# Kernel optimization log

Measured on AMD Instinct MI355X. Metric: run time of the kernel, lower is better.

The kernel has to match this reference:

```python
import jax, jax.numpy as jnp
import numpy as np

B, IN, N, OUT = 65536, 512, 256, 64  # batch, in_size, neurons, out_size


def setup_inputs() -> dict:
    key = jax.random.key(0)
    k1, k2, k3, k4 = jax.random.split(key, 4)
    return {
        "x": jax.random.normal(k1, (B, IN), jnp.float32),
        "W_lin": jax.random.normal(k2, (IN, N + OUT), jnp.float32),   # nlinear
        "W_nl": jax.random.normal(k3, (N - 1, N), jnp.float32),        # padded nonlinear[i] rows
        "W_out": jax.random.normal(k4, (OUT, N), jnp.float32),         # output_weights[0:out_size]
    }


def reference(x, W_lin, W_nl, W_out):
    act = jnp.tanh
    lin = x @ W_lin  # [B, N+OUT]
    # row i of nonlinear weights is valid only for entries 0..i (length i+1)
    tri_mask = (jnp.arange(N)[None, :] <= jnp.arange(N - 1)[:, None]).astype(lin.dtype)
    Wm = W_nl * tri_mask  # [N-1, N]
    # growing accumulator, fixed-size buffer; position 0 = lin[0] + 1
    acc0 = jnp.zeros((x.shape[0], N), lin.dtype).at[:, 0].set(lin[:, 0] + 1.0)
    col = jnp.arange(N)[None, :]

    def step(acc, inp):
        w, l, i = inp  # w: [N] masked weights, l: [B] = lin[:, i], i: scalar step
        v = jnp.sum(act(acc) * w[None, :], axis=1) + l + 1.0  # [B]
        acc = jnp.where(col == (i + 1), v[:, None], acc)
        return acc, None

    xs = (Wm, lin[:, : N - 1].T, jnp.arange(N - 1))
    acc, _ = jax.lax.scan(step, acc0, xs)
    # outs[i] = act(t) @ output_weights[i] + lin[neurons + i] + 1
    out = act(acc) @ W_out.T + lin[:, N:] + 1.0  # [B, OUT]
    return out
```

## Files before the change

kernel.cpp:

```cpp
#include <hip/hip_runtime.h>
#include <hip/hip_bf16.h>

typedef _Float16 f16x8 __attribute__((ext_vector_type(8)));
typedef unsigned short u16x8 __attribute__((ext_vector_type(8)));
typedef float f32x4 __attribute__((ext_vector_type(4)));
typedef unsigned int u32x4 __attribute__((ext_vector_type(4)));

static __device__ __forceinline__ unsigned short h2u(_Float16 h) {
    return __builtin_bit_cast(unsigned short, h);
}
static __device__ __forceinline__ float fast_tanh(float x) {
    float e = __expf(2.0f * x);
    return 1.0f - 2.0f / (e + 1.0f);
}

__global__ void cascade_prep(const float* __restrict__ W_lin,
                             const float* __restrict__ W_nl,
                             const float* __restrict__ W_out,
                             unsigned short* __restrict__ wlin_h,
                             unsigned short* __restrict__ wlin_l,
                             unsigned short* __restrict__ wnl_h,
                             unsigned short* __restrict__ wnl_l,
                             unsigned short* __restrict__ wout_h,
                             unsigned short* __restrict__ wout_l,
                             float* __restrict__ wcol) {
    int idx = blockIdx.x * blockDim.x + threadIdx.x;
    int stride = gridDim.x * blockDim.x;
    for (int i = idx; i < 320 * 512; i += stride) {
        int n = i >> 9, k = i & 511;
        float w = W_lin[k * 320 + n];
        _Float16 h = (_Float16)w;
        wlin_h[i] = h2u(h);
        wlin_l[i] = h2u((_Float16)(w - (float)h));
    }
    for (int i = idx; i < 255 * 256; i += stride) {
        int r = i >> 8, k = i & 255;
        float w = (k <= r) ? W_nl[i] : 0.0f;
        _Float16 h = (_Float16)w;
        wnl_h[i] = h2u(h);
        wnl_l[i] = h2u((_Float16)(w - (float)h));
    }
    for (int i = idx; i < 64 * 256; i += stride) {
        float w = W_out[i];
        _Float16 h = (_Float16)w;
        wout_h[i] = h2u(h);
        wout_l[i] = h2u((_Float16)(w - (float)h));
    }
    for (int i = idx; i < 256; i += stride) {
        int b = i >> 5, u = i & 31;
        float* dst = wcol + b * 496 + (31 * u - (u * (u - 1)) / 2);
        for (int j = u + 1; j < 32; ++j)
            dst[j - u - 1] = W_nl[(size_t)(b * 32 + j - 1) * 256 + b * 32 + u];
    }
}

__global__ __launch_bounds__(512, 1) void lin_gemm(
    const float* __restrict__ x,
    const unsigned short* __restrict__ wlin_h,
    const unsigned short* __restrict__ wlin_l,
    float* __restrict__ linc,
    float* __restrict__ lino) {

    __shared__ _Float16 bufH[2][16 * 520];
    __shared__ _Float16 bufL[2][16 * 520];

    const int tid = threadIdx.x;
    const int wv  = tid >> 6;
    const int l15 = tid & 15;
    const int g   = (tid & 63) >> 4;
    const int s = (blockIdx.x & 7) * 64 + (blockIdx.x >> 3);
    const long row0 = (long)s * 128;

    f16x8 xfh[16], xfl[16];
    {
        const float* xp = x + (row0 + wv * 16 + l15) * 512 + g * 8;
        #pragma unroll
        for (int ks = 0; ks < 16; ++ks) {
            float4 p0 = *reinterpret_cast<const float4*>(xp + ks * 32);
            float4 p1 = *reinterpret_cast<const float4*>(xp + ks * 32 + 4);
            float av[8] = {p0.x, p0.y, p0.z, p0.w, p1.x, p1.y, p1.z, p1.w};
            f16x8 fh, fl;
            #pragma unroll
            for (int e = 0; e < 8; ++e) {
                _Float16 hh = (_Float16)av[e];
                fh[e] = hh;
                fl[e] = (_Float16)(av[e] - (float)hh);
            }
            xfh[ks] = fh;
            xfl[ks] = fl;
        }
    }

    u16x8 rh[2], rl[2];
    #define STAGE_LOAD(nt)                                                     \
        {                                                                      \
            _Pragma("unroll")                                                  \
            for (int it = 0; it < 2; ++it) {                                   \
                int flat = it * 4096 + tid * 8;                                \
                int r = flat >> 9, c = flat & 511;                             \
                rh[it] = *reinterpret_cast<const u16x8*>(                      \
                    wlin_h + (size_t)((nt) * 16 + r) * 512 + c);               \
                rl[it] = *reinterpret_cast<const u16x8*>(                      \
                    wlin_l + (size_t)((nt) * 16 + r) * 512 + c);               \
            }                                                                  \
        }
    #define STAGE_WRITE(buf)                                                   \
        {                                                                      \
            _Pragma("unroll")                                                  \
            for (int it = 0; it < 2; ++it) {                                   \
                int flat = it * 4096 + tid * 8;                                \
                int r = flat >> 9, c = flat & 511;                             \
                *reinterpret_cast<u16x8*>(&bufH[buf][r * 520 + c]) =           \
                    __builtin_bit_cast(u16x8, rh[it]);                         \
                *reinterpret_cast<u16x8*>(&bufL[buf][r * 520 + c]) =           \
                    __builtin_bit_cast(u16x8, rl[it]);                         \
            }                                                                  \
        }

    STAGE_LOAD(0);
    STAGE_WRITE(0);
    __syncthreads();

    int cur = 0;
    for (int nt = 0; nt < 20; ++nt) {
        if (nt < 19) STAGE_LOAD(nt + 1);

        f32x4 acc = (f32x4){0.f, 0.f, 0.f, 0.f};
        if (nt < 16) {
            #pragma unroll
            for (int ks = 0; ks < 16; ++ks) {
                f16x8 bh = *reinterpret_cast<const f16x8*>(
                    &bufH[cur][l15 * 520 + ks * 32 + g * 8]);
                f16x8 bl = *reinterpret_cast<const f16x8*>(
                    &bufL[cur][l15 * 520 + ks * 32 + g * 8]);
                acc = __builtin_amdgcn_mfma_f32_16x16x32_f16(xfh[ks], bh, acc, 0, 0, 0);
                acc = __builtin_amdgcn_mfma_f32_16x16x32_f16(xfl[ks], bh, acc, 0, 0, 0);
                acc = __builtin_amdgcn_mfma_f32_16x16x32_f16(xfh[ks], bl, acc, 0, 0, 0);
            }
            int c = nt * 16 + l15;
            #pragma unroll
            for (int j = 0; j < 4; ++j) {
                long row = row0 + wv * 16 + g * 4 + j;
                if (c < 255) linc[row * 256 + c + 1] = acc[j];
                if (c == 0)  linc[row * 256] = acc[j];
            }
        } else {
            #pragma unroll
            for (int ks = 0; ks < 16; ++ks) {
                f16x8 bh = *reinterpret_cast<const f16x8*>(
                    &bufH[cur][l15 * 520 + ks * 32 + g * 8]);
                acc = __builtin_amdgcn_mfma_f32_16x16x32_f16(xfh[ks], bh, acc, 0, 0, 0);
            }
            #pragma unroll
            for (int j = 0; j < 4; ++j)
                lino[(row0 + wv * 16 + g * 4 + j) * 64 + (nt - 16) * 16 + l15] = acc[j];
        }

        if (nt < 19) STAGE_WRITE(cur ^ 1);
        __syncthreads();
        cur ^= 1;
    }
    #undef STAGE_LOAD
    #undef STAGE_WRITE
}

static __device__ __forceinline__ void unpack_pf(u32x4 a0, u32x4 a1,
                                                 f16x8* ah, f16x8* al) {
    u32x4 hx, lx;
    hx[0] = (a0[0] & 0xffffu) | (a0[1] << 16);
    hx[1] = (a0[2] & 0xffffu) | (a0[3] << 16);
    hx[2] = (a1[0] & 0xffffu) | (a1[1] << 16);
    hx[3] = (a1[2] & 0xffffu) | (a1[3] << 16);
    lx[0] = (a0[0] >> 16) | (a0[1] & 0xffff0000u);
    lx[1] = (a0[2] >> 16) | (a0[3] & 0xffff0000u);
    lx[2] = (a1[0] >> 16) | (a1[1] & 0xffff0000u);
    lx[3] = (a1[2] >> 16) | (a1[3] & 0xffff0000u);
    *ah = __builtin_bit_cast(f16x8, hx);
    *al = __builtin_bit_cast(f16x8, lx);
}

__global__ __launch_bounds__(64) void cascade_casc(
    const float* __restrict__ linc,
    const float* __restrict__ lino,
    const float* __restrict__ wcol,
    const unsigned short* __restrict__ wnl_h,
    const unsigned short* __restrict__ wnl_l,
    const unsigned short* __restrict__ wout_h,
    const unsigned short* __restrict__ wout_l,
    float* __restrict__ out) {

    __shared__ float conacc[16 * 260];
    __shared__ float wslab[500];
    unsigned int* conp = reinterpret_cast<unsigned int*>(conacc);

    const int l   = threadIdx.x;
    const int l15 = l & 15;
    const int g   = l >> 4;
    const int s = (blockIdx.x & 7) * 512 + (blockIdx.x >> 3);
    const long row0 = (long)s * 16;

    #pragma unroll
    for (int it = 0; it < 16; ++it) {
        int flat = it * 256 + l * 4;
        int rr = flat >> 8, c4 = flat & 255;
        float4 v = *reinterpret_cast<const float4*>(linc + (row0 + rr) * 256 + c4);
        *reinterpret_cast<float4*>(&conacc[rr * 260 + c4]) = v;
    }
    __syncthreads();

    #define NT_UPDATE(bs, nt, AH, AL)                                          \
        {                                                                      \
            const size_t wrow = (size_t)((nt) * 16 + l15 - 1) * 256            \
                                + (bs) * 32 + g * 8;                           \
            f16x8 bh_ = __builtin_bit_cast(f16x8,                              \
                *reinterpret_cast<const u16x8*>(wnl_h + wrow));                \
            f16x8 bl_ = __builtin_bit_cast(f16x8,                              \
                *reinterpret_cast<const u16x8*>(wnl_l + wrow));                \
            f32x4 d_ = (f32x4){0.f, 0.f, 0.f, 0.f};                            \
            d_ = __builtin_amdgcn_mfma_f32_16x16x32_f16(AH, bh_, d_, 0, 0, 0); \
            d_ = __builtin_amdgcn_mfma_f32_16x16x32_f16(AL, bh_, d_, 0, 0, 0); \
            d_ = __builtin_amdgcn_mfma_f32_16x16x32_f16(AH, bl_, d_, 0, 0, 0); \
            _Pragma("unroll")                                                  \
            for (int jj_ = 0; jj_ < 4; ++jj_) {                                \
                int idx_ = (g * 4 + jj_) * 260 + (nt) * 16 + l15;              \
                conacc[idx_] += d_[jj_];                                       \
            }                                                                  \
        }

    #pragma unroll
    for (int b = 0; b < 8; ++b) {
        {
            int i0 = l * 4;
            float4 v0 = *reinterpret_cast<const float4*>(wcol + b * 496 + i0);
            *reinterpret_cast<float4*>(&wslab[i0]) = v0;
            int i1 = 256 + l * 4;
            if (i1 < 496) {
                float4 v1 = *reinterpret_cast<const float4*>(wcol + b * 496 + i1);
                *reinterpret_cast<float4*>(&wslab[i1]) = v1;
            }
        }
        f16x8 pah = {}, pal = {};
        if (b >= 1) {
            const unsigned int* p = &conp[l15 * 260 + (b - 1) * 32 + g * 8];
            unpack_pf(*reinterpret_cast<const u32x4*>(p),
                      *reinterpret_cast<const u32x4*>(p + 4), &pah, &pal);
            NT_UPDATE(b - 1, 2 * b, pah, pal);
            NT_UPDATE(b - 1, 2 * b + 1, pah, pal);
        }
        __syncthreads();

        float acc[32];
        #pragma unroll
        for (int j = 0; j < 32; ++j) acc[j] = 0.0f;
        #pragma unroll
        for (int u8 = 0; u8 < 4; ++u8) {
            float4 cw0 = *reinterpret_cast<const float4*>(&conacc[l15 * 260 + b * 32 + u8 * 8]);
            float4 cw1 = *reinterpret_cast<const float4*>(&conacc[l15 * 260 + b * 32 + u8 * 8 + 4]);
            float conw[8] = {cw0.x, cw0.y, cw0.z, cw0.w, cw1.x, cw1.y, cw1.z, cw1.w};

            if (b >= 1) {
                #pragma unroll
                for (int q = 0; q < 3; ++q) {
                    const int nt = 2 * b + 2 + u8 * 3 + q;
                    if (nt < 16) NT_UPDATE(b - 1, nt, pah, pal);
                }
            }

            unsigned int pk[8];
            #pragma unroll
            for (int v = 0; v < 8; ++v) {
                const int u = u8 * 8 + v;
                float vv = acc[u] + conw[v] + 1.0f;
                float tv = fast_tanh(vv);
                _Float16 hv = (_Float16)tv;
                _Float16 lo = (_Float16)(tv - (float)hv);
                pk[v] = (unsigned int)h2u(hv) | ((unsigned int)h2u(lo) << 16);
                const float* wu = wslab + (31 * u - (u * (u - 1)) / 2);
                #pragma unroll
                for (int j = u + 1; j < 32; ++j)
                    acc[j] = fmaf(tv, wu[j - u - 1], acc[j]);
            }
            if (l < 16) {
                *reinterpret_cast<u32x4*>(&conp[l15 * 260 + b * 32 + u8 * 8]) =
                    (u32x4){pk[0], pk[1], pk[2], pk[3]};
                *reinterpret_cast<u32x4*>(&conp[l15 * 260 + b * 32 + u8 * 8 + 4]) =
                    (u32x4){pk[4], pk[5], pk[6], pk[7]};
            }
        }
        __syncthreads();
    }
    #undef NT_UPDATE

    #pragma unroll
    for (int n = 0; n < 4; ++n) {
        f32x4 acc = (f32x4){0.f, 0.f, 0.f, 0.f};
        #pragma unroll
        for (int kc = 0; kc < 8; ++kc) {
            const unsigned int* p = &conp[l15 * 260 + kc * 32 + g * 8];
            f16x8 ah, al;
            unpack_pf(*reinterpret_cast<const u32x4*>(p),
                      *reinterpret_cast<const u32x4*>(p + 4), &ah, &al);
            const size_t wrow = (size_t)(n * 16 + l15) * 256 + kc * 32 + g * 8;
            f16x8 bh = __builtin_bit_cast(f16x8, *reinterpret_cast<const u16x8*>(wout_h + wrow));
            f16x8 bl = __builtin_bit_cast(f16x8, *reinterpret_cast<const u16x8*>(wout_l + wrow));
            acc = __builtin_amdgcn_mfma_f32_16x16x32_f16(ah, bh, acc, 0, 0, 0);
            acc = __builtin_amdgcn_mfma_f32_16x16x32_f16(al, bh, acc, 0, 0, 0);
            acc = __builtin_amdgcn_mfma_f32_16x16x32_f16(ah, bl, acc, 0, 0, 0);
        }
        #pragma unroll
        for (int j = 0; j < 4; ++j) {
            long rr = row0 + g * 4 + j;
            int c = n * 16 + l15;
            out[rr * 64 + c] = acc[j] + lino[rr * 64 + c] + 1.0f;
        }
    }
}

extern "C" void kernel_launch(void* const* d_in, const int* in_sizes, int n_in,
                              void* d_out, int out_size, void* d_ws, size_t ws_size,
                              hipStream_t stream) {
    (void)in_sizes; (void)n_in; (void)out_size; (void)ws_size;
    const float* x     = (const float*)d_in[0];
    const float* W_lin = (const float*)d_in[1];
    const float* W_nl  = (const float*)d_in[2];
    const float* W_out = (const float*)d_in[3];
    float* out = (float*)d_out;

    char* ws = (char*)d_ws;
    unsigned short* wlin_h = (unsigned short*)(ws);
    unsigned short* wlin_l = (unsigned short*)(ws + 327680);
    unsigned short* wnl_h  = (unsigned short*)(ws + 916480);
    unsigned short* wnl_l  = (unsigned short*)(ws + 1047040);
    unsigned short* wout_h = (unsigned short*)(ws + 1177600);
    unsigned short* wout_l = (unsigned short*)(ws + 1210368);
    float*          wcol   = (float*)(ws + 1243136);
    float*          linc   = (float*)(ws + 1259008);
    float*          lino   = (float*)(ws + 68367872);

    cascade_prep<<<256, 256, 0, stream>>>(W_lin, W_nl, W_out,
                                          wlin_h, wlin_l, wnl_h, wnl_l,
                                          wout_h, wout_l, wcol);
    lin_gemm<<<512, 512, 0, stream>>>(x, wlin_h, wlin_l, linc, lino);
    cascade_casc<<<4096, 64, 0, stream>>>(linc, lino, wcol,
                                          wnl_h, wnl_l, wout_h, wout_l, out);
}
```

Baseline: 232.3 us.

## Split cascade kernel into serial-chain wave and MFMA update wave

The cascade kernel now runs two wavefronts per block. Wave 0 handles the serial tanh/FMA chain within each 32-neuron block and stages the column weights. Wave 1 does the MFMA trailing updates for later neuron tiles, and the two waves split the output GEMM tiles between them. The aim is to overlap the latency-bound serial chain with the matrix-core updates. The cost is that wave 1 now does all of its trailing updates before the barrier instead of interleaving them, and each block uses twice the threads.

```diff
diff --git a/kernel.cpp b/kernel.cpp
--- a/kernel.cpp
+++ b/kernel.cpp
@@ -179,7 +179,7 @@
     *al = __builtin_bit_cast(f16x8, lx);
 }
 
-__global__ __launch_bounds__(64) void cascade_casc(
+__global__ __launch_bounds__(128) void cascade_casc(
     const float* __restrict__ linc,
     const float* __restrict__ lino,
     const float* __restrict__ wcol,
@@ -193,15 +193,17 @@
     __shared__ float wslab[500];
     unsigned int* conp = reinterpret_cast<unsigned int*>(conacc);
 
-    const int l   = threadIdx.x;
-    const int l15 = l & 15;
-    const int g   = l >> 4;
+    const int tid = threadIdx.x;
+    const int wv  = tid >> 6;
+    const int ll  = tid & 63;
+    const int l15 = ll & 15;
+    const int g   = ll >> 4;
     const int s = (blockIdx.x & 7) * 512 + (blockIdx.x >> 3);
     const long row0 = (long)s * 16;
 
     #pragma unroll
-    for (int it = 0; it < 16; ++it) {
-        int flat = it * 256 + l * 4;
+    for (int it = 0; it < 8; ++it) {
+        int flat = it * 512 + tid * 4;
         int rr = flat >> 8, c4 = flat & 255;
         float4 v = *reinterpret_cast<const float4*>(linc + (row0 + rr) * 256 + c4);
         *reinterpret_cast<float4*>(&conacc[rr * 260 + c4]) = v;
@@ -229,18 +231,19 @@
 
     #pragma unroll
     for (int b = 0; b < 8; ++b) {
-        {
-            int i0 = l * 4;
-            float4 v0 = *reinterpret_cast<const float4*>(wcol + b * 496 + i0);
-            *reinterpret_cast<float4*>(&wslab[i0]) = v0;
-            int i1 = 256 + l * 4;
+        f16x8 pah = {}, pal = {};
+        if (wv == 0) {
+            int i0 = ll * 4;
+            if (i0 < 496) {
+                float4 v0 = *reinterpret_cast<const float4*>(wcol + b * 496 + i0);
+                *reinterpret_cast<float4*>(&wslab[i0]) = v0;
+            }
+            int i1 = 256 + ll * 4;
             if (i1 < 496) {
                 float4 v1 = *reinterpret_cast<const float4*>(wcol + b * 496 + i1);
                 *reinterpret_cast<float4*>(&wslab[i1]) = v1;
             }
-        }
-        f16x8 pah = {}, pal = {};
-        if (b >= 1) {
+        } else if (b >= 1) {
             const unsigned int* p = &conp[l15 * 260 + (b - 1) * 32 + g * 8];
             unpack_pf(*reinterpret_cast<const u32x4*>(p),
                       *reinterpret_cast<const u32x4*>(p + 4), &pah, &pal);
@@ -249,50 +252,47 @@
         }
         __syncthreads();
 
-        float acc[32];
-        #pragma unroll
-        for (int j = 0; j < 32; ++j) acc[j] = 0.0f;
-        #pragma unroll
-        for (int u8 = 0; u8 < 4; ++u8) {
-            float4 cw0 = *reinterpret_cast<const float4*>(&conacc[l15 * 260 + b * 32 + u8 * 8]);
-            float4 cw1 = *reinterpret_cast<const float4*>(&conacc[l15 * 260 + b * 32 + u8 * 8 + 4]);
-            float conw[8] = {cw0.x, cw0.y, cw0.z, cw0.w, cw1.x, cw1.y, cw1.z, cw1.w};
-
-            if (b >= 1) {
+        if (wv == 0) {
+            float acc[32];
+            #pragma unroll
+            for (int j = 0; j < 32; ++j) acc[j] = 0.0f;
+            #pragma unroll
+            for (int u8 = 0; u8 < 4; ++u8) {
+                float4 cw0 = *reinterpret_cast<const float4*>(&conacc[l15 * 260 + b * 32 + u8 * 8]);
+                float4 cw1 = *reinterpret_cast<const float4*>(&conacc[l15 * 260 + b * 32 + u8 * 8 + 4]);
+                float conw[8] = {cw0.x, cw0.y, cw0.z, cw0.w, cw1.x, cw1.y, cw1.z, cw1.w};
+                unsigned int pk[8];
                 #pragma unroll
-                for (int q = 0; q < 3; ++q) {
-                    const int nt = 2 * b + 2 + u8 * 3 + q;
-                    if (nt < 16) NT_UPDATE(b - 1, nt, pah, pal);
+                for (int v = 0; v < 8; ++v) {
+                    const int u = u8 * 8 + v;
+                    float vv = acc[u] + conw[v] + 1.0f;
+                    float tv = fast_tanh(vv);
+                    _Float16 hv = (_Float16)tv;
+                    _Float16 lo = (_Float16)(tv - (float)hv);
+                    pk[v] = (unsigned int)h2u(hv) | ((unsigned int)h2u(lo) << 16);
+                    const float* wu = wslab + (31 * u - (u * (u - 1)) / 2);
+                    #pragma unroll
+                    for (int j = u + 1; j < 32; ++j)
+                        acc[j] = fmaf(tv, wu[j - u - 1], acc[j]);
                 }
-            }
-
-            unsigned int pk[8];
-            #pragma unroll
-            for (int v = 0; v < 8; ++v) {
-                const int u = u8 * 8 + v;
-                float vv = acc[u] + conw[v] + 1.0f;
-                float tv = fast_tanh(vv);
-                _Float16 hv = (_Float16)tv;
-                _Float16 lo = (_Float16)(tv - (float)hv);
-                pk[v] = (unsigned int)h2u(hv) | ((unsigned int)h2u(lo) << 16);
-                const float* wu = wslab + (31 * u - (u * (u - 1)) / 2);
-                #pragma unroll
-                for (int j = u + 1; j < 32; ++j)
-                    acc[j] = fmaf(tv, wu[j - u - 1], acc[j]);
-            }
-            if (l < 16) {
-                *reinterpret_cast<u32x4*>(&conp[l15 * 260 + b * 32 + u8 * 8]) =
-                    (u32x4){pk[0], pk[1], pk[2], pk[3]};
-                *reinterpret_cast<u32x4*>(&conp[l15 * 260 + b * 32 + u8 * 8 + 4]) =
-                    (u32x4){pk[4], pk[5], pk[6], pk[7]};
-            }
+                if (ll < 16) {
+                    *reinterpret_cast<u32x4*>(&conp[l15 * 260 + b * 32 + u8 * 8]) =
+                        (u32x4){pk[0], pk[1], pk[2], pk[3]};
+                    *reinterpret_cast<u32x4*>(&conp[l15 * 260 + b * 32 + u8 * 8 + 4]) =
+                        (u32x4){pk[4], pk[5], pk[6], pk[7]};
+                }
+            }
+        } else if (b >= 1) {
+            for (int nt = 2 * b + 2; nt < 16; ++nt)
+                NT_UPDATE(b - 1, nt, pah, pal);
         }
         __syncthreads();
     }
     #undef NT_UPDATE
 
     #pragma unroll
-    for (int n = 0; n < 4; ++n) {
+    for (int nn = 0; nn < 2; ++nn) {
+        const int n = wv * 2 + nn;
         f32x4 acc = (f32x4){0.f, 0.f, 0.f, 0.f};
         #pragma unroll
         for (int kc = 0; kc < 8; ++kc) {
@@ -341,6 +341,6 @@
                                           wlin_h, wlin_l, wnl_h, wnl_l,
                                           wout_h, wout_l, wcol);
     lin_gemm<<<512, 512, 0, stream>>>(x, wlin_h, wlin_l, linc, lino);
-    cascade_casc<<<4096, 64, 0, stream>>>(linc, lino, wcol,
-                                          wnl_h, wnl_l, wout_h, wout_l, out);
-}
+    cascade_casc<<<4096, 128, 0, stream>>>(linc, lino, wcol,
+                                           wnl_h, wnl_l, wout_h, wout_l, out);
+}
```

New measurement: 461.1 us. 1.99x slower.
